# Kernel tuning notes

Measured on AMD Instinct MI355X. Metric: run time of the kernel, lower is better.

Reference implementation:

```python
import jax, jax.numpy as jnp
import numpy as np

N_NODES = 40000
N_EDGES = 640000
D_IN = 128
D_OUT = 128


def setup_inputs() -> dict:
    key = jax.random.key(0)
    k1, k2, k3, k4, k5 = jax.random.split(key, 5)
    feature = jax.random.normal(k1, (N_NODES, D_IN), dtype=jnp.float32)
    src_idx = jax.random.randint(k2, (N_EDGES,), 0, N_NODES, dtype=jnp.int64)
    dst_idx = jax.random.randint(k3, (N_EDGES,), 0, N_NODES, dtype=jnp.int64)
    W = jax.random.normal(k4, (D_OUT, D_IN), dtype=jnp.float32) * (1.0 / np.sqrt(D_IN))
    b = jax.random.normal(k5, (D_OUT,), dtype=jnp.float32) * 0.01
    return {"feature": feature, "src_idx": src_idx, "dst_idx": dst_idx, "W": W, "b": b}


def reference(feature, src_idx, dst_idx, W, b):
    # u_mul_v: per-edge message = x[src] * x[dst]   [E, D]
    msg = feature[src_idx] * feature[dst_idx]
    # mean aggregation at destination nodes (nodes with no in-edges get 0, like DGL)
    summed = jax.ops.segment_sum(msg, dst_idx, num_segments=N_NODES)  # [N, D]
    cnt = jax.ops.segment_sum(jnp.ones((msg.shape[0],), dtype=feature.dtype),
                              dst_idx, num_segments=N_NODES)  # [N]
    x = summed / jnp.maximum(cnt, 1.0)[:, None]
    # final linear: x @ W.T + b
    return x @ W.T + b
```

## Files before the change

### kernel.cpp

```cpp
#include <hip/hip_runtime.h>

#define N_NODES 40000
#define N_EDGES 640000
#define D 128
#define CAP 64
#define PREP_GRID 2560
#define XPITCH 132

typedef __attribute__((ext_vector_type(8))) short short8;
typedef __attribute__((ext_vector_type(4))) float float4v;

static __device__ __forceinline__ unsigned bf16_rne(float f) {
    unsigned u = __float_as_uint(f);
    return (u + 0x7FFFu + ((u >> 16) & 1u)) >> 16;
}
static __device__ __forceinline__ unsigned pack2(float a, float b) {
    return bf16_rne(a) | (bf16_rne(b) << 16);
}

__global__ __launch_bounds__(256) void prep_kernel(
    const float* __restrict__ feat,
    const int*   __restrict__ src,
    const int*   __restrict__ dst,
    const float* __restrict__ W,
    unsigned*    __restrict__ featb,
    unsigned*    __restrict__ wfrag,
    int*         __restrict__ deg,
    int*         __restrict__ bucket)
{
    const int g  = blockIdx.x * 256 + threadIdx.x;
    const int GT = PREP_GRID * 256;

    for (int i = g; i < N_NODES * D / 4; i += GT) {
        float4 f = reinterpret_cast<const float4*>(feat)[i];
        uint2 p;
        p.x = pack2(f.x, f.y);
        p.y = pack2(f.z, f.w);
        reinterpret_cast<uint2*>(featb)[i] = p;
    }

    if (g < 32 * 64) {
        const int tile = g >> 6, lane = g & 63;
        const int nt = tile >> 2, kt = tile & 3;
        const int n = nt * 16 + (lane & 15);
        const int k = kt * 32 + (lane >> 4) * 8;
        const float* wp = W + (size_t)n * D + k;
        uint4 p;
        p.x = pack2(wp[0], wp[1]);
        p.y = pack2(wp[2], wp[3]);
        p.z = pack2(wp[4], wp[5]);
        p.w = pack2(wp[6], wp[7]);
        reinterpret_cast<uint4*>(wfrag)[g] = p;
    }

    for (int e = g; e < N_EDGES; e += GT) {
        int d = dst[e];
        int r = atomicAdd(&deg[d], 1);
        if (r < CAP) bucket[d * CAP + r] = src[e];
    }
}

__global__ __launch_bounds__(256) void agg_gemm(
    const float*    __restrict__ feat,
    const unsigned* __restrict__ featb,
    const unsigned* __restrict__ wfrag,
    const int*      __restrict__ deg,
    const int*      __restrict__ bucket,
    const float*    __restrict__ bias,
    float*          __restrict__ out)
{
    __shared__ float xs[16 * XPITCH];
    const int t     = threadIdx.x;
    const int wave  = t >> 6;
    const int lane  = t & 63;
    const int node0 = blockIdx.x * 16;

    #pragma unroll
    for (int k = 0; k < 4; ++k) {
        const int n  = node0 + wave * 4 + k;
        const int dg = min(deg[n], CAP);
        const int* __restrict__ bl = bucket + n * CAP;

        float2 acc = make_float2(0.f, 0.f);
        int i = 0;
        for (; i + 3 < dg; i += 4) {
            unsigned v0 = featb[(size_t)bl[i]     * (D / 2) + lane];
            unsigned v1 = featb[(size_t)bl[i + 1] * (D / 2) + lane];
            unsigned v2 = featb[(size_t)bl[i + 2] * (D / 2) + lane];
            unsigned v3 = featb[(size_t)bl[i + 3] * (D / 2) + lane];
            acc.x += (__uint_as_float(v0 << 16) + __uint_as_float(v1 << 16)) +
                     (__uint_as_float(v2 << 16) + __uint_as_float(v3 << 16));
            acc.y += (__uint_as_float(v0 & 0xFFFF0000u) + __uint_as_float(v1 & 0xFFFF0000u)) +
                     (__uint_as_float(v2 & 0xFFFF0000u) + __uint_as_float(v3 & 0xFFFF0000u));
        }
        for (; i < dg; ++i) {
            unsigned v0 = featb[(size_t)bl[i] * (D / 2) + lane];
            acc.x += __uint_as_float(v0 << 16);
            acc.y += __uint_as_float(v0 & 0xFFFF0000u);
        }

        const float2 fd = reinterpret_cast<const float2*>(feat + (size_t)n * D)[lane];
        const float inv = 1.0f / (float)max(dg, 1);
        acc.x *= fd.x * inv;
        acc.y *= fd.y * inv;
        xs[(wave * 4 + k) * XPITCH + lane * 2]     = acc.x;
        xs[(wave * 4 + k) * XPITCH + lane * 2 + 1] = acc.y;
    }
    __syncthreads();

    {
        const int arow = lane & 15;
        const int aq   = lane >> 4;
        const int col  = lane & 15;

        short8 afrag[4];
        #pragma unroll
        for (int kt = 0; kt < 4; ++kt) {
            const float* xp = xs + arow * XPITCH + kt * 32 + aq * 8;
            union { short8 s; unsigned u[4]; } af;
            af.u[0] = pack2(xp[0], xp[1]);
            af.u[1] = pack2(xp[2], xp[3]);
            af.u[2] = pack2(xp[4], xp[5]);
            af.u[3] = pack2(xp[6], xp[7]);
            afrag[kt] = af.s;
        }

        float4v acc[2];
        #pragma unroll
        for (int nt2 = 0; nt2 < 2; ++nt2) {
            float b = bias[(wave * 2 + nt2) * 16 + col];
            acc[nt2] = (float4v){b, b, b, b};
        }

        #pragma unroll
        for (int kt = 0; kt < 4; ++kt) {
            #pragma unroll
            for (int nt2 = 0; nt2 < 2; ++nt2) {
                const int tile = (wave * 2 + nt2) * 4 + kt;
                union { short8 s; uint4 u; } bf;
                bf.u = reinterpret_cast<const uint4*>(wfrag)[tile * 64 + lane];
                acc[nt2] = __builtin_amdgcn_mfma_f32_16x16x32_bf16(
                    afrag[kt], bf.s, acc[nt2], 0, 0, 0);
            }
        }

        const int rbase = (lane >> 4) * 4;
        #pragma unroll
        for (int nt2 = 0; nt2 < 2; ++nt2) {
            const int c = (wave * 2 + nt2) * 16 + col;
            #pragma unroll
            for (int r = 0; r < 4; ++r)
                out[(size_t)(node0 + rbase + r) * D + c] = acc[nt2][r];
        }
    }
}

extern "C" void kernel_launch(void* const* d_in, const int* in_sizes, int n_in,
                              void* d_out, int out_size, void* d_ws, size_t ws_size,
                              hipStream_t stream)
{
    const float* feat = (const float*)d_in[0];
    const int*   src  = (const int*)  d_in[1];
    const int*   dst  = (const int*)  d_in[2];
    const float* W    = (const float*)d_in[3];
    const float* bias = (const float*)d_in[4];
    float* out = (float*)d_out;

    unsigned* featb  = (unsigned*)d_ws;
    unsigned* wfrag  = featb + (size_t)N_NODES * D / 2;
    int*      bucket = (int*)(wfrag + 8192);
    int*      deg    = bucket + (size_t)N_NODES * CAP;

    hipMemsetAsync(deg, 0, N_NODES * sizeof(int), stream);
    prep_kernel<<<PREP_GRID, 256, 0, stream>>>(feat, src, dst, W, featb, wfrag, deg, bucket);
    agg_gemm<<<N_NODES / 16, 256, 0, stream>>>(feat, featb, wfrag, deg, bucket, bias, out);
}
```

Before: 152.7 us.

## Store bucket indices as 16-bit, broadcast via shuffle, widen aggregation blocks

Bucket source indices are stored as unsigned short, which halves bucket traffic. Each wave loads a node's whole index list in one coalesced read and hands indices out with __shfl instead of loading them one at a time. The aggregation kernel moves to 512 threads per block, with 2 nodes per wave and one MFMA column tile per wave, and gathers 8 neighbours at a time. The edge bucketing loop now runs first in prep. Indices above 65535 would be truncated; that is safe here because N_NODES is 40000.

```diff
diff --git a/kernel.cpp b/kernel.cpp
--- a/kernel.cpp
+++ b/kernel.cpp
@@ -23,13 +23,19 @@
     const int*   __restrict__ src,
     const int*   __restrict__ dst,
     const float* __restrict__ W,
-    unsigned*    __restrict__ featb,
-    unsigned*    __restrict__ wfrag,
-    int*         __restrict__ deg,
-    int*         __restrict__ bucket)
+    unsigned*       __restrict__ featb,
+    unsigned*       __restrict__ wfrag,
+    int*            __restrict__ deg,
+    unsigned short* __restrict__ bucket)
 {
     const int g  = blockIdx.x * 256 + threadIdx.x;
     const int GT = PREP_GRID * 256;
+
+    for (int e = g; e < N_EDGES; e += GT) {
+        int d = dst[e];
+        int r = atomicAdd(&deg[d], 1);
+        if (r < CAP) bucket[(size_t)d * CAP + r] = (unsigned short)src[e];
+    }
 
     for (int i = g; i < N_NODES * D / 4; i += GT) {
         float4 f = reinterpret_cast<const float4*>(feat)[i];
@@ -52,22 +58,16 @@
         p.w = pack2(wp[6], wp[7]);
         reinterpret_cast<uint4*>(wfrag)[g] = p;
     }
-
-    for (int e = g; e < N_EDGES; e += GT) {
-        int d = dst[e];
-        int r = atomicAdd(&deg[d], 1);
-        if (r < CAP) bucket[d * CAP + r] = src[e];
-    }
 }
 
-__global__ __launch_bounds__(256) void agg_gemm(
-    const float*    __restrict__ feat,
-    const unsigned* __restrict__ featb,
-    const unsigned* __restrict__ wfrag,
-    const int*      __restrict__ deg,
-    const int*      __restrict__ bucket,
-    const float*    __restrict__ bias,
-    float*          __restrict__ out)
+__global__ __launch_bounds__(512) void agg_gemm(
+    const float*          __restrict__ feat,
+    const unsigned*       __restrict__ featb,
+    const unsigned*       __restrict__ wfrag,
+    const int*            __restrict__ deg,
+    const unsigned short* __restrict__ bucket,
+    const float*          __restrict__ bias,
+    float*                __restrict__ out)
 {
     __shared__ float xs[16 * XPITCH];
     const int t     = threadIdx.x;
@@ -75,26 +75,38 @@
     const int lane  = t & 63;
     const int node0 = blockIdx.x * 16;
 
+    const int n0  = node0 + wave * 2;
+    const int dg0 = min(deg[n0],     CAP);
+    const int dg1 = min(deg[n0 + 1], CAP);
+    const unsigned iw0 = reinterpret_cast<const unsigned*>(bucket + (size_t)n0 * CAP)[lane & 31];
+    const unsigned iw1 = reinterpret_cast<const unsigned*>(bucket + (size_t)(n0 + 1) * CAP)[lane & 31];
+
     #pragma unroll
-    for (int k = 0; k < 4; ++k) {
-        const int n  = node0 + wave * 4 + k;
-        const int dg = min(deg[n], CAP);
-        const int* __restrict__ bl = bucket + n * CAP;
+    for (int k = 0; k < 2; ++k) {
+        const int dg = k ? dg1 : dg0;
+        const unsigned iw = k ? iw1 : iw0;
+        const int n = n0 + k;
 
         float2 acc = make_float2(0.f, 0.f);
         int i = 0;
-        for (; i + 3 < dg; i += 4) {
-            unsigned v0 = featb[(size_t)bl[i]     * (D / 2) + lane];
-            unsigned v1 = featb[(size_t)bl[i + 1] * (D / 2) + lane];
-            unsigned v2 = featb[(size_t)bl[i + 2] * (D / 2) + lane];
-            unsigned v3 = featb[(size_t)bl[i + 3] * (D / 2) + lane];
-            acc.x += (__uint_as_float(v0 << 16) + __uint_as_float(v1 << 16)) +
-                     (__uint_as_float(v2 << 16) + __uint_as_float(v3 << 16));
-            acc.y += (__uint_as_float(v0 & 0xFFFF0000u) + __uint_as_float(v1 & 0xFFFF0000u)) +
-                     (__uint_as_float(v2 & 0xFFFF0000u) + __uint_as_float(v3 & 0xFFFF0000u));
+        for (; i + 7 < dg; i += 8) {
+            unsigned v[8];
+            #pragma unroll
+            for (int j = 0; j < 8; ++j) {
+                int word = __shfl((int)iw, (i + j) >> 1, 64);
+                int idx  = ((i + j) & 1) ? ((word >> 16) & 0xFFFF) : (word & 0xFFFF);
+                v[j] = featb[(size_t)idx * (D / 2) + lane];
+            }
+            #pragma unroll
+            for (int j = 0; j < 8; ++j) {
+                acc.x += __uint_as_float(v[j] << 16);
+                acc.y += __uint_as_float(v[j] & 0xFFFF0000u);
+            }
         }
         for (; i < dg; ++i) {
-            unsigned v0 = featb[(size_t)bl[i] * (D / 2) + lane];
+            int word = __shfl((int)iw, i >> 1, 64);
+            int idx  = (i & 1) ? ((word >> 16) & 0xFFFF) : (word & 0xFFFF);
+            unsigned v0 = featb[(size_t)idx * (D / 2) + lane];
             acc.x += __uint_as_float(v0 << 16);
             acc.y += __uint_as_float(v0 & 0xFFFF0000u);
         }
@@ -103,8 +115,8 @@
         const float inv = 1.0f / (float)max(dg, 1);
         acc.x *= fd.x * inv;
         acc.y *= fd.y * inv;
-        xs[(wave * 4 + k) * XPITCH + lane * 2]     = acc.x;
-        xs[(wave * 4 + k) * XPITCH + lane * 2 + 1] = acc.y;
+        xs[(wave * 2 + k) * XPITCH + lane * 2]     = acc.x;
+        xs[(wave * 2 + k) * XPITCH + lane * 2 + 1] = acc.y;
     }
     __syncthreads();
 
@@ -125,33 +137,21 @@
             afrag[kt] = af.s;
         }
 
-        float4v acc[2];
-        #pragma unroll
-        for (int nt2 = 0; nt2 < 2; ++nt2) {
-            float b = bias[(wave * 2 + nt2) * 16 + col];
-            acc[nt2] = (float4v){b, b, b, b};
-        }
+        float bo = bias[wave * 16 + col];
+        float4v acc = (float4v){bo, bo, bo, bo};
 
         #pragma unroll
         for (int kt = 0; kt < 4; ++kt) {
-            #pragma unroll
-            for (int nt2 = 0; nt2 < 2; ++nt2) {
-                const int tile = (wave * 2 + nt2) * 4 + kt;
-                union { short8 s; uint4 u; } bf;
-                bf.u = reinterpret_cast<const uint4*>(wfrag)[tile * 64 + lane];
-                acc[nt2] = __builtin_amdgcn_mfma_f32_16x16x32_bf16(
-                    afrag[kt], bf.s, acc[nt2], 0, 0, 0);
-            }
+            union { short8 s; uint4 u; } bf;
+            bf.u = reinterpret_cast<const uint4*>(wfrag)[(wave * 4 + kt) * 64 + lane];
+            acc = __builtin_amdgcn_mfma_f32_16x16x32_bf16(afrag[kt], bf.s, acc, 0, 0, 0);
         }
 
         const int rbase = (lane >> 4) * 4;
+        const int c = wave * 16 + col;
         #pragma unroll
-        for (int nt2 = 0; nt2 < 2; ++nt2) {
-            const int c = (wave * 2 + nt2) * 16 + col;
-            #pragma unroll
-            for (int r = 0; r < 4; ++r)
-                out[(size_t)(node0 + rbase + r) * D + c] = acc[nt2][r];
-        }
+        for (int r = 0; r < 4; ++r)
+            out[(size_t)(node0 + rbase + r) * D + c] = acc[r];
     }
 }
 
@@ -166,12 +166,12 @@
     const float* bias = (const float*)d_in[4];
     float* out = (float*)d_out;
 
-    unsigned* featb  = (unsigned*)d_ws;
-    unsigned* wfrag  = featb + (size_t)N_NODES * D / 2;
-    int*      bucket = (int*)(wfrag + 8192);
-    int*      deg    = bucket + (size_t)N_NODES * CAP;
+    unsigned*       featb  = (unsigned*)d_ws;
+    unsigned*       wfrag  = featb + (size_t)N_NODES * D / 2;
+    unsigned short* bucket = (unsigned short*)(wfrag + 8192);
+    int*            deg    = (int*)(bucket + (size_t)N_NODES * CAP);
 
     hipMemsetAsync(deg, 0, N_NODES * sizeof(int), stream);
     prep_kernel<<<PREP_GRID, 256, 0, stream>>>(feat, src, dst, W, featb, wfrag, deg, bucket);
-    agg_gemm<<<N_NODES / 16, 256, 0, stream>>>(feat, featb, wfrag, deg, bucket, bias, out);
+    agg_gemm<<<N_NODES / 16, 512, 0, stream>>>(feat, featb, wfrag, deg, bucket, bias, out);
 }
```

Measured after the change: 144.6 us. 5.3% less time.
